# Kernel tuning notes

Hardware: AMD Instinct MI355X
Metric: run time of the kernel (lower is better)

## Reference

```python
import jax, jax.numpy as jnp
import numpy as np

B, T, D, H = 8, 4096, 1024, 1024


def setup_inputs() -> dict:
    key = jax.random.key(0)
    ks = jax.random.split(key, 8)
    s = 1.0 / np.sqrt(D)
    x = jax.random.normal(ks[0], (B, T, D), dtype=jnp.float32)
    Wq = jax.random.uniform(ks[1], (H, D), jnp.float32, -s, s)
    bq = jax.random.uniform(ks[2], (H,), jnp.float32, -s, s)
    Wk = jax.random.uniform(ks[3], (H, D), jnp.float32, -s, s)
    bk = jax.random.uniform(ks[4], (H,), jnp.float32, -s, s)
    Wv = jax.random.uniform(ks[5], (H, D), jnp.float32, -s, s)
    bv = jax.random.uniform(ks[6], (H,), jnp.float32, -s, s)
    wbias = jax.random.uniform(ks[7], (H,), jnp.float32, 0.0, 1.0)  # torch.rand
    return {"x": x, "Wq": Wq, "bq": bq, "Wk": Wk, "bk": bk, "Wv": Wv, "bv": bv, "wbias": wbias}


def reference(x, Wq, bq, Wk, bk, Wv, bv, wbias):
    # Q, K, V: [B, T, H]
    Q = jnp.einsum('btd,hd->bth', x, Wq) + bq
    K = jnp.einsum('btd,hd->bth', x, Wk) + bk
    V = jnp.einsum('btd,hd->bth', x, Wv) + bv
    Q_sig = jax.nn.sigmoid(Q)
    numer = jnp.exp(K + wbias)            # [B, T, H]
    denom = numer.sum(axis=0)             # [T, H] (faithful: sum over batch axis)
    weighted = (numer * V).sum(axis=0) / denom  # [T, H]
    Yt = Q_sig * weighted                 # broadcast -> [B, T, H]
    return Yt  # to_out is Identity since dim == hidden_dim
```

## Files before the change

kernel.cpp:

```cpp
#include <hip/hip_runtime.h>
#include <hip/hip_bf16.h>

#define B_ 8
#define T_ 4096
#define D_ 1024
#define H_ 1024

typedef __attribute__((ext_vector_type(8))) short short8;
typedef __attribute__((ext_vector_type(4))) float floatx4;

#define GLOAD16(gptr, lptr) \
  __builtin_amdgcn_global_load_lds((const __attribute__((address_space(1))) void*)(gptr), \
                                   (__attribute__((address_space(3))) void*)(lptr), 16, 0, 0)

__device__ __forceinline__ ushort f2b(float f) {
  unsigned x = __builtin_bit_cast(unsigned, f);
  unsigned r = (x + 0x7fffu + ((x >> 16) & 1u)) >> 16;
  return (ushort)r;
}

__global__ void cvt_kernel(const float* __restrict__ in, ushort* __restrict__ out, int n) {
  int idx = blockIdx.x * blockDim.x + threadIdx.x;
  int stride = gridDim.x * blockDim.x;
  for (long i = (long)idx * 8; i < n; i += (long)stride * 8) {
    const float4 f0 = *(const float4*)(in + i);
    const float4 f1 = *(const float4*)(in + i + 4);
    union { ushort u[8]; uint4 v; } r;
    r.u[0] = f2b(f0.x); r.u[1] = f2b(f0.y); r.u[2] = f2b(f0.z); r.u[3] = f2b(f0.w);
    r.u[4] = f2b(f1.x); r.u[5] = f2b(f1.y); r.u[6] = f2b(f1.z); r.u[7] = f2b(f1.w);
    *(uint4*)(out + i) = r.v;
  }
}

__global__ __launch_bounds__(512, 2) void kv_kernel(
    const ushort* __restrict__ xb, const ushort* __restrict__ Wkb,
    const ushort* __restrict__ Wvb, const float* __restrict__ bk,
    const float* __restrict__ bv, const float* __restrict__ wbias,
    float* __restrict__ weighted) {
  extern __shared__ ushort lds[];
  ushort* const AsB = lds;
  ushort* const KsB = lds + 49152;
  ushort* const VsB = lds + 61440;

  const int tid = threadIdx.x;
  const int lane = tid & 63;
  const int w = tid >> 6;
  const int wrow = w >> 1;
  const int wcol = w & 1;
  const int t0 = blockIdx.x * 256;
  const int h0 = blockIdx.y * 64;

  const int srow = tid >> 3;
  const int swz = (tid & 7) ^ ((tid >> 3) & 7);

  const int arow = wrow * 64 + (lane & 15);
  const int bcol = wcol * 32 + (lane & 15);
  const int cs0 = (lane >> 4) ^ (lane & 7);
  const int cs1 = ((lane >> 4) + 4) ^ (lane & 7);

  float wbc[2], bkc[2], bvc[2];
#pragma unroll
  for (int n = 0; n < 2; ++n) {
    int h = h0 + wcol * 32 + n * 16 + (lane & 15);
    wbc[n] = wbias[h];
    bkc[n] = bk[h];
    bvc[n] = bv[h];
  }

  const ushort* xsb = xb + (size_t)(t0 + srow) * D_ + swz * 8;
  const ushort* ksb = Wkb + (size_t)(h0 + srow) * D_ + swz * 8;
  const ushort* vsb = Wvb + (size_t)(h0 + srow) * D_ + swz * 8;

  auto stage = [&](int p, int nb) {
    const int b = p >> 4;
    const int kt = (p & 15) << 6;
    const ushort* xs = xsb + (size_t)b * (T_ * D_) + kt;
    ushort* Ab = AsB + nb * 16384;
#pragma unroll
    for (int it = 0; it < 4; ++it)
      GLOAD16(xs + (size_t)(it * 64) * D_, Ab + (it * 512 + tid) * 8);
    GLOAD16(ksb + kt, KsB + nb * 4096 + tid * 8);
    GLOAD16(vsb + kt, VsB + nb * 4096 + tid * 8);
  };

  floatx4 accK[4][2] = {};
  floatx4 accV[4][2] = {};
  floatx4 sumN[4][2] = {};
  floatx4 sumWV[4][2] = {};

  stage(0, 0);
  stage(1, 1);
  asm volatile("s_waitcnt vmcnt(6)" ::: "memory");
  __builtin_amdgcn_s_barrier();

  int cur = 0, stg = 2;
  for (int p = 0; p < 128; ++p) {
    if (p < 126) stage(p + 2, stg);

    const ushort* Ac = AsB + cur * 16384;
    const ushort* Kc = KsB + cur * 4096;
    const ushort* Vc = VsB + cur * 4096;
#pragma unroll
    for (int s = 0; s < 2; ++s) {
      const int cs = s ? cs1 : cs0;
      short8 a[4], kb2[2], vb2[2];
#pragma unroll
      for (int m = 0; m < 4; ++m)
        a[m] = *(const short8*)&Ac[(arow + m * 16) * 64 + cs * 8];
#pragma unroll
      for (int n = 0; n < 2; ++n) {
        kb2[n] = *(const short8*)&Kc[(bcol + n * 16) * 64 + cs * 8];
        vb2[n] = *(const short8*)&Vc[(bcol + n * 16) * 64 + cs * 8];
      }
      __builtin_amdgcn_s_setprio(1);
#pragma unroll
      for (int m = 0; m < 4; ++m)
#pragma unroll
        for (int n = 0; n < 2; ++n) {
          accK[m][n] = __builtin_amdgcn_mfma_f32_16x16x32_bf16(a[m], kb2[n], accK[m][n], 0, 0, 0);
          accV[m][n] = __builtin_amdgcn_mfma_f32_16x16x32_bf16(a[m], vb2[n], accV[m][n], 0, 0, 0);
        }
      __builtin_amdgcn_s_setprio(0);
    }

    if ((p & 15) == 15) {
#pragma unroll
      for (int m = 0; m < 4; ++m)
#pragma unroll
        for (int n = 0; n < 2; ++n) {
#pragma unroll
          for (int r = 0; r < 4; ++r) {
            float nmr = __expf(accK[m][n][r] + bkc[n] + wbc[n]);
            sumN[m][n][r] += nmr;
            sumWV[m][n][r] += nmr * (accV[m][n][r] + bvc[n]);
          }
          accK[m][n] = floatx4{0.f, 0.f, 0.f, 0.f};
          accV[m][n] = floatx4{0.f, 0.f, 0.f, 0.f};
        }
    }

    if (p < 126) { asm volatile("s_waitcnt vmcnt(6)" ::: "memory"); }
    else         { asm volatile("s_waitcnt vmcnt(0)" ::: "memory"); }
    __builtin_amdgcn_s_barrier();
    cur = (cur == 2) ? 0 : cur + 1;
    stg = (stg == 2) ? 0 : stg + 1;
  }

#pragma unroll
  for (int m = 0; m < 4; ++m)
#pragma unroll
    for (int n = 0; n < 2; ++n)
#pragma unroll
      for (int r = 0; r < 4; ++r) {
        int t = t0 + wrow * 64 + m * 16 + (lane >> 4) * 4 + r;
        int h = h0 + wcol * 32 + n * 16 + (lane & 15);
        weighted[(size_t)t * H_ + h] = sumWV[m][n][r] / sumN[m][n][r];
      }
}

__global__ __launch_bounds__(512, 2) void q_kernel(
    const ushort* __restrict__ xb, const ushort* __restrict__ Wqb,
    const float* __restrict__ bq, const float* __restrict__ weighted,
    float* __restrict__ out) {
  extern __shared__ ushort lds[];
  ushort* const AsB = lds;
  ushort* const BsB = lds + 24576;

  const int tid = threadIdx.x;
  const int lane = tid & 63;
  const int w = tid >> 6;
  const int wrow = w >> 1;
  const int wcol = w & 1;
  const int R0 = blockIdx.x * 256;
  const int h0 = blockIdx.y * 128;

  const int srow = tid >> 2;
  const int sq = (tid & 3) ^ ((tid >> 3) & 3);

  const int arow = wrow * 64 + (lane & 15);
  const int brow = wcol * 64 + (lane & 15);
  const int cq = (lane >> 4) ^ (((lane & 15) >> 1) & 3);

  const ushort* xsrc = xb + (size_t)(R0 + srow) * D_ + sq * 8;
  const ushort* wsrc = Wqb + (size_t)(h0 + srow) * D_ + sq * 8;

  auto stage = [&](int kt, int nb) {
    GLOAD16(xsrc + kt, AsB + nb * 8192 + tid * 8);
    GLOAD16(xsrc + (size_t)128 * D_ + kt, AsB + nb * 8192 + (tid + 512) * 8);
    GLOAD16(wsrc + kt, BsB + nb * 4096 + tid * 8);
  };

  floatx4 acc[4][4] = {};

  stage(0, 0);
  stage(32, 1);
  asm volatile("s_waitcnt vmcnt(3)" ::: "memory");
  __builtin_amdgcn_s_barrier();

  int cur = 0, stg = 2;
  for (int it = 0; it < 32; ++it) {
    if (it < 30) stage((it + 2) * 32, stg);

    const ushort* Ac = AsB + cur * 8192;
    const ushort* Bc = BsB + cur * 4096;
    short8 a[4], bb[4];
#pragma unroll
    for (int m = 0; m < 4; ++m)
      a[m] = *(const short8*)&Ac[(arow + m * 16) * 32 + cq * 8];
#pragma unroll
    for (int n = 0; n < 4; ++n)
      bb[n] = *(const short8*)&Bc[(brow + n * 16) * 32 + cq * 8];
    __builtin_amdgcn_s_setprio(1);
#pragma unroll
    for (int m = 0; m < 4; ++m)
#pragma unroll
      for (int n = 0; n < 4; ++n)
        acc[m][n] = __builtin_amdgcn_mfma_f32_16x16x32_bf16(a[m], bb[n], acc[m][n], 0, 0, 0);
    __builtin_amdgcn_s_setprio(0);

    if (it < 30) { asm volatile("s_waitcnt vmcnt(3)" ::: "memory"); }
    else         { asm volatile("s_waitcnt vmcnt(0)" ::: "memory"); }
    __builtin_amdgcn_s_barrier();
    cur = (cur == 2) ? 0 : cur + 1;
    stg = (stg == 2) ? 0 : stg + 1;
  }

  float bqc[4];
#pragma unroll
  for (int n = 0; n < 4; ++n)
    bqc[n] = bq[h0 + wcol * 64 + n * 16 + (lane & 15)];

#pragma unroll
  for (int m = 0; m < 4; ++m)
#pragma unroll
    for (int n = 0; n < 4; ++n)
#pragma unroll
      for (int r = 0; r < 4; ++r) {
        int row = R0 + wrow * 64 + m * 16 + (lane >> 4) * 4 + r;
        int t = row & (T_ - 1);
        int h = h0 + wcol * 64 + n * 16 + (lane & 15);
        float q = acc[m][n][r] + bqc[n];
        float sig = 1.f / (1.f + __expf(-q));
        out[(size_t)row * H_ + h] = sig * weighted[(size_t)t * H_ + h];
      }
}

extern "C" void kernel_launch(void* const* d_in, const int* in_sizes, int n_in,
                              void* d_out, int out_size, void* d_ws, size_t ws_size,
                              hipStream_t stream) {
  (void)in_sizes; (void)n_in; (void)out_size; (void)ws_size;
  const float* x = (const float*)d_in[0];
  const float* Wq = (const float*)d_in[1];
  const float* bq = (const float*)d_in[2];
  const float* Wk = (const float*)d_in[3];
  const float* bk = (const float*)d_in[4];
  const float* Wv = (const float*)d_in[5];
  const float* bv = (const float*)d_in[6];
  const float* wbias = (const float*)d_in[7];
  float* out = (float*)d_out;

  char* ws = (char*)d_ws;
  const size_t XN = (size_t)B_ * T_ * D_;
  const size_t WN = (size_t)H_ * D_;
  ushort* xb  = (ushort*)ws;
  ushort* Wqb = (ushort*)(ws + XN * 2);
  ushort* Wkb = Wqb + WN;
  ushort* Wvb = Wkb + WN;
  float* weighted = (float*)(ws + XN * 2 + 3 * WN * 2);

  (void)hipFuncSetAttribute((const void*)kv_kernel,
                            hipFuncAttributeMaxDynamicSharedMemorySize, 147456);
  (void)hipFuncSetAttribute((const void*)q_kernel,
                            hipFuncAttributeMaxDynamicSharedMemorySize, 73728);

  cvt_kernel<<<2048, 256, 0, stream>>>(x, xb, (int)XN);
  cvt_kernel<<<512, 256, 0, stream>>>(Wq, Wqb, (int)WN);
  cvt_kernel<<<512, 256, 0, stream>>>(Wk, Wkb, (int)WN);
  cvt_kernel<<<512, 256, 0, stream>>>(Wv, Wvb, (int)WN);

  kv_kernel<<<dim3(T_ / 256, H_ / 64), 512, 147456, stream>>>(xb, Wkb, Wvb, bk, bv, wbias, weighted);
  q_kernel<<<dim3((B_ * T_) / 256, H_ / 128), 512, 73728, stream>>>(xb, Wqb, bq, weighted, out);
}
```

Measured before the change: 285.0 us.

## Enlarge Q GEMM tile, remap blocks for XCD locality, coalesce epilogue via LDS

The Q kernel moves from 256x128 tiles to 256x256 tiles with a 4-deep LDS ring and 8x4 MFMA accumulators per wave, which raises arithmetic intensity per loaded byte. Its epilogue now stages accumulators through LDS so the sigmoid-times-weighted output and the weighted reads are done as coalesced float4 accesses. Both GEMM kernels switch to a 1D grid whose block ids are remapped so neighbouring tiles land on the same XCD for L2 reuse. The three weight conversions are merged into one launch. In exchange, more registers and 128KB of LDS per block may reduce occupancy.

```diff
diff --git a/kernel.cpp b/kernel.cpp
--- a/kernel.cpp
+++ b/kernel.cpp
@@ -32,6 +32,22 @@
   }
 }
 
+__global__ void cvt3_kernel(const float* __restrict__ w0, const float* __restrict__ w1,
+                            const float* __restrict__ w2, ushort* __restrict__ out, int n) {
+  const float* in = (blockIdx.y == 0) ? w0 : (blockIdx.y == 1) ? w1 : w2;
+  ushort* o = out + (size_t)blockIdx.y * n;
+  int idx = blockIdx.x * blockDim.x + threadIdx.x;
+  int stride = gridDim.x * blockDim.x;
+  for (long i = (long)idx * 8; i < n; i += (long)stride * 8) {
+    const float4 f0 = *(const float4*)(in + i);
+    const float4 f1 = *(const float4*)(in + i + 4);
+    union { ushort u[8]; uint4 v; } r;
+    r.u[0] = f2b(f0.x); r.u[1] = f2b(f0.y); r.u[2] = f2b(f0.z); r.u[3] = f2b(f0.w);
+    r.u[4] = f2b(f1.x); r.u[5] = f2b(f1.y); r.u[6] = f2b(f1.z); r.u[7] = f2b(f1.w);
+    *(uint4*)(o + i) = r.v;
+  }
+}
+
 __global__ __launch_bounds__(512, 2) void kv_kernel(
     const ushort* __restrict__ xb, const ushort* __restrict__ Wkb,
     const ushort* __restrict__ Wvb, const float* __restrict__ bk,
@@ -47,8 +63,11 @@
   const int w = tid >> 6;
   const int wrow = w >> 1;
   const int wcol = w & 1;
-  const int t0 = blockIdx.x * 256;
-  const int h0 = blockIdx.y * 64;
+
+  const int bid = blockIdx.x;
+  const int lid = (bid & 7) * 32 + (bid >> 3);
+  const int t0 = (lid >> 4) * 256;
+  const int h0 = (lid & 15) * 64;
 
   const int srow = tid >> 3;
   const int swz = (tid & 7) ^ ((tid >> 3) & 7);
@@ -159,90 +178,100 @@
 }
 
 __global__ __launch_bounds__(512, 2) void q_kernel(
-    const ushort* __restrict__ xb, const ushort* __restrict__ Wqb,
+    const ushort* __restrict__ Am, const ushort* __restrict__ Bm,
     const float* __restrict__ bq, const float* __restrict__ weighted,
     float* __restrict__ out) {
   extern __shared__ ushort lds[];
-  ushort* const AsB = lds;
-  ushort* const BsB = lds + 24576;
 
   const int tid = threadIdx.x;
   const int lane = tid & 63;
   const int w = tid >> 6;
-  const int wrow = w >> 1;
-  const int wcol = w & 1;
-  const int R0 = blockIdx.x * 256;
-  const int h0 = blockIdx.y * 128;
-
-  const int srow = tid >> 2;
-  const int sq = (tid & 3) ^ ((tid >> 3) & 3);
-
-  const int arow = wrow * 64 + (lane & 15);
-  const int brow = wcol * 64 + (lane & 15);
-  const int cq = (lane >> 4) ^ (((lane & 15) >> 1) & 3);
-
-  const ushort* xsrc = xb + (size_t)(R0 + srow) * D_ + sq * 8;
-  const ushort* wsrc = Wqb + (size_t)(h0 + srow) * D_ + sq * 8;
-
-  auto stage = [&](int kt, int nb) {
-    GLOAD16(xsrc + kt, AsB + nb * 8192 + tid * 8);
-    GLOAD16(xsrc + (size_t)128 * D_ + kt, AsB + nb * 8192 + (tid + 512) * 8);
-    GLOAD16(wsrc + kt, BsB + nb * 4096 + tid * 8);
+  const int wr = w >> 2;
+  const int wc = w & 3;
+
+  const int bid = blockIdx.x;
+  const int lid = (bid & 7) * 64 + (bid >> 3);
+  const int R0 = (lid >> 2) * 256;
+  const int C0 = (lid & 3) * 256;
+
+  const int r0 = tid >> 2;
+  const int lc = (tid & 3) ^ ((tid >> 3) & 3);
+  const ushort* asrc = Am + (size_t)(R0 + r0) * D_ + lc * 8;
+  const ushort* bsrc = Bm + (size_t)(C0 + r0) * D_ + lc * 8;
+
+  auto stage = [&](int t) {
+    const int nb = t & 3;
+    const int kt = t * 32;
+    GLOAD16(asrc + kt, lds + nb * 8192 + tid * 8);
+    GLOAD16(asrc + kt + (size_t)128 * D_, lds + nb * 8192 + (512 + tid) * 8);
+    GLOAD16(bsrc + kt, lds + 32768 + nb * 8192 + tid * 8);
+    GLOAD16(bsrc + kt + (size_t)128 * D_, lds + 32768 + nb * 8192 + (512 + tid) * 8);
   };
 
-  floatx4 acc[4][4] = {};
-
-  stage(0, 0);
-  stage(32, 1);
-  asm volatile("s_waitcnt vmcnt(3)" ::: "memory");
+  const int baseA = wr * 128 + (lane & 15);
+  const int baseB = wc * 64 + (lane & 15);
+  const int aOff = baseA * 32 + ((lane >> 4) ^ ((baseA >> 1) & 3)) * 8;
+  const int bOff = baseB * 32 + ((lane >> 4) ^ ((baseB >> 1) & 3)) * 8;
+
+  floatx4 acc[8][4] = {};
+
+  stage(0); stage(1);
+  asm volatile("s_waitcnt vmcnt(4)" ::: "memory");
   __builtin_amdgcn_s_barrier();
 
-  int cur = 0, stg = 2;
-  for (int it = 0; it < 32; ++it) {
-    if (it < 30) stage((it + 2) * 32, stg);
-
-    const ushort* Ac = AsB + cur * 8192;
-    const ushort* Bc = BsB + cur * 4096;
-    short8 a[4], bb[4];
-#pragma unroll
-    for (int m = 0; m < 4; ++m)
-      a[m] = *(const short8*)&Ac[(arow + m * 16) * 32 + cq * 8];
-#pragma unroll
-    for (int n = 0; n < 4; ++n)
-      bb[n] = *(const short8*)&Bc[(brow + n * 16) * 32 + cq * 8];
-    __builtin_amdgcn_s_setprio(1);
-#pragma unroll
-    for (int m = 0; m < 4; ++m)
+  const int NT = D_ / 32;
+  for (int t = 0; t < NT; ++t) {
+    if (t < NT - 2) stage(t + 2);
+    const ushort* Ab = lds + (t & 3) * 8192;
+    const ushort* Bb = lds + 32768 + (t & 3) * 8192;
+
+    short8 b[4], a[8];
+#pragma unroll
+    for (int n = 0; n < 4; ++n) b[n] = *(const short8*)(Bb + bOff + n * 512);
+#pragma unroll
+    for (int m = 0; m < 8; ++m) a[m] = *(const short8*)(Ab + aOff + m * 512);
+#pragma unroll
+    for (int m = 0; m < 8; ++m)
 #pragma unroll
       for (int n = 0; n < 4; ++n)
-        acc[m][n] = __builtin_amdgcn_mfma_f32_16x16x32_bf16(a[m], bb[n], acc[m][n], 0, 0, 0);
-    __builtin_amdgcn_s_setprio(0);
-
-    if (it < 30) { asm volatile("s_waitcnt vmcnt(3)" ::: "memory"); }
-    else         { asm volatile("s_waitcnt vmcnt(0)" ::: "memory"); }
+        acc[m][n] = __builtin_amdgcn_mfma_f32_16x16x32_bf16(a[m], b[n], acc[m][n], 0, 0, 0);
+
+    if (t < NT - 2) { asm volatile("s_waitcnt vmcnt(4)" ::: "memory"); }
+    else            { asm volatile("s_waitcnt vmcnt(0)" ::: "memory"); }
     __builtin_amdgcn_s_barrier();
-    cur = (cur == 2) ? 0 : cur + 1;
-    stg = (stg == 2) ? 0 : stg + 1;
-  }
-
-  float bqc[4];
-#pragma unroll
-  for (int n = 0; n < 4; ++n)
-    bqc[n] = bq[h0 + wcol * 64 + n * 16 + (lane & 15)];
-
-#pragma unroll
-  for (int m = 0; m < 4; ++m)
-#pragma unroll
-    for (int n = 0; n < 4; ++n)
-#pragma unroll
-      for (int r = 0; r < 4; ++r) {
-        int row = R0 + wrow * 64 + m * 16 + (lane >> 4) * 4 + r;
-        int t = row & (T_ - 1);
-        int h = h0 + wcol * 64 + n * 16 + (lane & 15);
-        float q = acc[m][n][r] + bqc[n];
-        float sig = 1.f / (1.f + __expf(-q));
-        out[(size_t)row * H_ + h] = sig * weighted[(size_t)t * H_ + h];
-      }
+  }
+
+  const int lrb = wr * 64 + (lane >> 4) * 4;
+  const int lcol = wc * 64 + (lane & 15);
+#pragma unroll
+  for (int mh = 0; mh < 2; ++mh) {
+    if (mh) __builtin_amdgcn_s_barrier();
+    float* lf = (float*)lds;
+#pragma unroll
+    for (int mi = 0; mi < 4; ++mi)
+#pragma unroll
+      for (int n = 0; n < 4; ++n)
+#pragma unroll
+        for (int r = 0; r < 4; ++r)
+          lf[(lrb + mi * 16 + r) * 256 + lcol + n * 16] = acc[mh * 4 + mi][n][r];
+    __builtin_amdgcn_s_barrier();
+#pragma unroll
+    for (int j = 0; j < 16; ++j) {
+      int cidx = j * 512 + tid;
+      int lr = cidx >> 6;
+      int cc = cidx & 63;
+      int grow = R0 + (lr >> 6) * 128 + mh * 64 + (lr & 63);
+      float4 v = *(float4*)(lf + lr * 256 + cc * 4);
+      float4 bq4 = *(const float4*)(bq + C0 + cc * 4);
+      float4 wv = *(const float4*)(weighted + (size_t)(grow & (T_ - 1)) * H_ + C0 + cc * 4);
+      float4 o;
+      o.x = wv.x / (1.f + __expf(-(v.x + bq4.x)));
+      o.y = wv.y / (1.f + __expf(-(v.y + bq4.y)));
+      o.z = wv.z / (1.f + __expf(-(v.z + bq4.z)));
+      o.w = wv.w / (1.f + __expf(-(v.w + bq4.w)));
+      *(float4*)(out + (size_t)grow * H_ + C0 + cc * 4) = o;
+    }
+  }
 }
 
 extern "C" void kernel_launch(void* const* d_in, const int* in_sizes, int n_in,
@@ -271,13 +300,11 @@
   (void)hipFuncSetAttribute((const void*)kv_kernel,
                             hipFuncAttributeMaxDynamicSharedMemorySize, 147456);
   (void)hipFuncSetAttribute((const void*)q_kernel,
-                            hipFuncAttributeMaxDynamicSharedMemorySize, 73728);
+                            hipFuncAttributeMaxDynamicSharedMemorySize, 131072);
 
   cvt_kernel<<<2048, 256, 0, stream>>>(x, xb, (int)XN);
-  cvt_kernel<<<512, 256, 0, stream>>>(Wq, Wqb, (int)WN);
-  cvt_kernel<<<512, 256, 0, stream>>>(Wk, Wkb, (int)WN);
-  cvt_kernel<<<512, 256, 0, stream>>>(Wv, Wvb, (int)WN);
-
-  kv_kernel<<<dim3(T_ / 256, H_ / 64), 512, 147456, stream>>>(xb, Wkb, Wvb, bk, bv, wbias, weighted);
-  q_kernel<<<dim3((B_ * T_) / 256, H_ / 128), 512, 73728, stream>>>(xb, Wqb, bq, weighted, out);
-}
+  cvt3_kernel<<<dim3(512, 3), 256, 0, stream>>>(Wq, Wk, Wv, Wqb, (int)WN);
+
+  kv_kernel<<<256, 512, 147456, stream>>>(xb, Wkb, Wvb, bk, bv, wbias, weighted);
+  q_kernel<<<512, 512, 131072, stream>>>(xb, Wqb, bq, weighted, out);
+}
```

Result: faster. 276.9 us (-2.9%).
